# Kernel optimization log

Measured on AMD Instinct MI355X. Metric: run time of the kernel, lower is better.

Reference implementation:

```python
import jax, jax.numpy as jnp
import numpy as np

# KernelConv config (pinned by hard-coded views in the source)
KS = [1, 3, 5, 7]          # sorted kernel sizes
KTOT = sum(KS)             # 16
KMAX = KS[-1]              # 7
COLOR = 4                  # packed Bayer channels
RGB = 3
H = W = 48                 # hard-coded in source view


def setup_inputs() -> dict:
    key = jax.random.key(0)
    k1, k2, k3 = jax.random.split(key, 3)
    B, N = 4, 8
    frames = jax.random.normal(k1, (B, N, COLOR, H, W), dtype=jnp.float32)
    # core channels = N * 2*KTOT * COLOR * RGB = 8 * 32 * 12 = 3072
    core = jax.random.normal(k2, (B, N * 2 * KTOT * COLOR * RGB, H, W), dtype=jnp.float32)
    kernel_weight = jax.random.uniform(k3, (B, N, len(KS), RGB, H, W), dtype=jnp.float32)
    return {"frames": frames, "core": core, "kernel_weight": kernel_weight}


def _kernel_conv(frames, core, kernel_weight):
    B, N, color, h, w = frames.shape
    # --- _sep_conv_core: separable 1D cores -> 2D per-pixel cores (outer product) ---
    c = core.reshape(B, N, 2 * KTOT, color, RGB, h, w)
    c1, c2 = c[:, :, :KTOT], c[:, :, KTOT:]
    cores = {}
    cur = 0
    for K in KS:
        t1 = c1[:, :, cur:cur + K]          # [B,N,K,color,3,h,w]
        t2 = c2[:, :, cur:cur + K]
        # outer product over the two kernel axes (torch einsum ijklcnop,ijlmcnop->ijkmcnop)
        cores[K] = jnp.einsum('bnkcthw,bnlcthw->bnklcthw', t1, t2)  # [B,N,K,K,color,3,h,w]
        cur += K
    # --- pad all kernels to KMAX and stack (reversed kernel order, as in source) ---
    padded = []
    for K in KS[::-1]:
        p = (KMAX - K) // 2
        padded.append(jnp.pad(cores[K], ((0, 0), (0, 0), (p, p), (p, p), (0, 0), (0, 0), (0, 0), (0, 0))))
    pk = jnp.stack(padded, axis=2)                              # [B,N,S,KMAX,KMAX,color,3,h,w]
    pk = pk.reshape(B, N, len(KS), KMAX * KMAX * color, RGB, h, w)
    # weighted fusion across kernel scales
    wk = jnp.mean(pk * kernel_weight[:, :, :, None], axis=2)    # [B,N,KMAX^2*color,3,h,w]
    # --- img_stack: KMAX^2 shifted views of the padded frames ---
    r = KMAX // 2
    fpad = jnp.pad(frames, ((0, 0), (0, 0), (0, 0), (r, r), (r, r)))
    shifts = [fpad[..., i:i + h, j:j + w] for i in range(KMAX) for j in range(KMAX)]
    img_stack = jnp.stack(shifts, axis=2)                       # [B,N,KMAX^2,color,h,w]
    # --- per-pixel conv: sum over kernel taps and color for each RGB output ---
    wk_r = wk.reshape(B, N, KMAX * KMAX, color, RGB, h, w)
    pred_img_i = jnp.einsum('bnkcthw,bnkchw->bnthw', wk_r, img_stack)  # [B,N,3,h,w]
    pred_img = jnp.mean(pred_img_i, axis=1)                            # [B,3,h,w]
    return pred_img_i, pred_img


def reference(frames, core, kernel_weight):
    return _kernel_conv(frames, core, kernel_weight)
```

## Files before the change

kernel.cpp:

```cpp
#include <hip/hip_runtime.h>

#define HH 48
#define WW 48
#define HW 2304
#define NB 8
#define CB 4
#define TB 3

__global__ __launch_bounds__(256) void kconv_fused(
    const float* __restrict__ frames,
    const float* __restrict__ core,
    const float* __restrict__ kw,
    float* __restrict__ out)
{
    const int blk = blockIdx.x;
    const int pc  = blk % (HW / 64);
    int rem = blk / (HW / 64);
    const int t = rem % TB; rem /= TB;
    const int n = rem % NB;
    const int b = rem / NB;
    const int tix = threadIdx.x;
    const int c   = tix >> 6;
    const int p64 = tix & 63;
    const int pix = pc * 64 + p64;
    const int x = pix % WW;
    const int y = pix / WW;

    const float* cp = core + ((size_t)b * 3072 + (size_t)((n * 32) * CB + c) * 3 + t) * HW + pix;

    float bv[16];
    #pragma unroll
    for (int q = 0; q < 16; ++q)
        bv[q] = cp[(size_t)((q + 16) * 12) * HW];

    int   xoff[7];
    float xmsk[7];
    #pragma unroll
    for (int j = 0; j < 7; ++j) {
        const int xx = x + j - 3;
        xoff[j] = min(max(xx, 0), WW - 1);
        xmsk[j] = ((xx >= 0) & (xx < WW)) ? 1.f : 0.f;
    }

    const float* fb = frames + ((size_t)(b * NB + n) * CB + c) * HW;

    float in7[7], in5[5], in3[3], f1 = 0.f;
    #pragma unroll
    for (int i = 0; i < 7; ++i) {
        const int yy = y + i - 3;
        const float ymsk = ((yy >= 0) & (yy < HH)) ? 1.f : 0.f;
        const float* frow = fb + min(max(yy, 0), HH - 1) * WW;
        float fp[7];
        #pragma unroll
        for (int j = 0; j < 7; ++j)
            fp[j] = frow[xoff[j]] * (ymsk * xmsk[j]);
        float s7 = 0.f;
        #pragma unroll
        for (int j = 0; j < 7; ++j) s7 = fmaf(bv[9 + j], fp[j], s7);
        in7[i] = s7;
        if (i >= 1 && i <= 5) {
            float s5 = 0.f;
            #pragma unroll
            for (int j = 0; j < 5; ++j) s5 = fmaf(bv[4 + j], fp[1 + j], s5);
            in5[i - 1] = s5;
        }
        if (i >= 2 && i <= 4) {
            float s3 = 0.f;
            #pragma unroll
            for (int j = 0; j < 3; ++j) s3 = fmaf(bv[1 + j], fp[2 + j], s3);
            in3[i - 2] = s3;
        }
        if (i == 3) f1 = bv[0] * fp[3];
    }

    __builtin_amdgcn_sched_barrier(0);

    float a[16];
    #pragma unroll
    for (int q = 0; q < 16; ++q)
        a[q] = cp[(size_t)(q * 12) * HW];

    const float* kwp = kw + ((size_t)(b * NB + n) * 12 + t) * HW + pix;
    const float kw0 = kwp[0];
    const float kw1 = kwp[(size_t)3 * HW];
    const float kw2 = kwp[(size_t)6 * HW];
    const float kw3 = kwp[(size_t)9 * HW];

    float r7 = 0.f, r5 = 0.f, r3 = 0.f;
    #pragma unroll
    for (int i = 0; i < 7; ++i) r7 = fmaf(a[9 + i], in7[i], r7);
    #pragma unroll
    for (int i = 0; i < 5; ++i) r5 = fmaf(a[4 + i], in5[i], r5);
    #pragma unroll
    for (int i = 0; i < 3; ++i) r3 = fmaf(a[1 + i], in3[i], r3);
    const float r1 = a[0] * f1;

    const float val = fmaf(kw0, r7, fmaf(kw1, r5, fmaf(kw2, r3, kw3 * r1)));

    __shared__ float lds[CB][64];
    lds[c][p64] = val;
    __syncthreads();
    if (tix < 64) {
        const float s = lds[0][tix] + lds[1][tix] + lds[2][tix] + lds[3][tix];
        out[((size_t)(b * NB + n) * TB + t) * HW + pc * 64 + tix] = 0.25f * s;
    }
}

__global__ __launch_bounds__(256) void mean_fb(
    const float* __restrict__ pii, float* __restrict__ pm)
{
    const int tid = blockIdx.x * blockDim.x + threadIdx.x;
    if (tid >= 4 * TB * HW) return;
    const int pix3 = tid % (TB * HW);
    const int b = tid / (TB * HW);
    float s = 0.f;
    #pragma unroll
    for (int n = 0; n < NB; ++n)
        s += pii[(size_t)((b * NB + n) * TB) * HW + pix3];
    pm[tid] = s * 0.125f;
}

extern "C" void kernel_launch(void* const* d_in, const int* in_sizes, int n_in,
                              void* d_out, int out_size, void* d_ws, size_t ws_size,
                              hipStream_t stream) {
    const float* frames = (const float*)d_in[0];
    const float* core   = (const float*)d_in[1];
    const float* kw     = (const float*)d_in[2];
    float* out = (float*)d_out;
    float* pm  = out + 4 * NB * TB * HW;

    kconv_fused<<<4 * NB * TB * (HW / 64), 256, 0, stream>>>(frames, core, kw, out);
    mean_fb<<<(4 * TB * HW + 255) / 256, 256, 0, stream>>>(out, pm);
}
```

Before: 27.28 us.

## Fuse conv and frame-mean into one cooperative kernel with grid sync

```diff
diff --git a/kernel.cpp b/kernel.cpp
--- a/kernel.cpp
+++ b/kernel.cpp
@@ -1,4 +1,7 @@
 #include <hip/hip_runtime.h>
+#include <hip/hip_cooperative_groups.h>
+
+namespace cg = cooperative_groups;
 
 #define HH 48
 #define WW 48
@@ -6,22 +9,19 @@
 #define NB 8
 #define CB 4
 #define TB 3
+#define NCHUNK (4 * NB * TB * (HW / 64))
 
-__global__ __launch_bounds__(256) void kconv_fused(
-    const float* __restrict__ frames,
-    const float* __restrict__ core,
-    const float* __restrict__ kw,
-    float* __restrict__ out)
+
+__device__ __forceinline__ void do_chunk(
+    const float* __restrict__ frames, const float* __restrict__ core,
+    const float* __restrict__ kw, float* __restrict__ out,
+    int blk, int tix, int c, int p64, float lds[CB][64])
 {
-    const int blk = blockIdx.x;
-    const int pc  = blk % (HW / 64);
+    const int pc = blk % (HW / 64);
     int rem = blk / (HW / 64);
     const int t = rem % TB; rem /= TB;
     const int n = rem % NB;
     const int b = rem / NB;
-    const int tix = threadIdx.x;
-    const int c   = tix >> 6;
-    const int p64 = tix & 63;
     const int pix = pc * 64 + p64;
     const int x = pix % WW;
     const int y = pix / WW;
@@ -97,13 +97,48 @@
 
     const float val = fmaf(kw0, r7, fmaf(kw1, r5, fmaf(kw2, r3, kw3 * r1)));
 
-    __shared__ float lds[CB][64];
     lds[c][p64] = val;
     __syncthreads();
     if (tix < 64) {
-        const float s = lds[0][tix] + lds[1][tix] + lds[2][tix] + lds[3][tix];
-        out[((size_t)(b * NB + n) * TB + t) * HW + pc * 64 + tix] = 0.25f * s;
+        const float s4 = 0.25f * (lds[0][tix] + lds[1][tix] + lds[2][tix] + lds[3][tix]);
+        out[((size_t)(b * NB + n) * TB + t) * HW + pc * 64 + tix] = s4;
     }
+    __syncthreads();
+}
+
+__global__ __launch_bounds__(256) void kconv_coop(
+    const float* __restrict__ frames, const float* __restrict__ core,
+    const float* __restrict__ kw, float* __restrict__ out, float* __restrict__ pm)
+{
+    const int tix = threadIdx.x;
+    const int c   = tix >> 6;
+    const int p64 = tix & 63;
+    __shared__ float lds[CB][64];
+
+    for (int blk = blockIdx.x; blk < NCHUNK; blk += gridDim.x)
+        do_chunk(frames, core, kw, out, blk, tix, c, p64, lds);
+
+    cg::this_grid().sync();
+
+    for (int tid = blockIdx.x * blockDim.x + tix; tid < 4 * TB * HW;
+         tid += gridDim.x * blockDim.x) {
+        const int pix3 = tid % (TB * HW);
+        const int b = tid / (TB * HW);
+        float s = 0.f;
+        #pragma unroll
+        for (int n = 0; n < NB; ++n)
+            s += out[(size_t)((b * NB + n) * TB) * HW + pix3];
+        pm[tid] = s * 0.125f;
+    }
+}
+
+__global__ __launch_bounds__(256) void kconv_fused(
+    const float* __restrict__ frames, const float* __restrict__ core,
+    const float* __restrict__ kw, float* __restrict__ out)
+{
+    const int tix = threadIdx.x;
+    __shared__ float lds[CB][64];
+    do_chunk(frames, core, kw, out, blockIdx.x, tix, tix >> 6, tix & 63, lds);
 }
 
 __global__ __launch_bounds__(256) void mean_fb(
@@ -127,8 +162,22 @@
     const float* core   = (const float*)d_in[1];
     const float* kw     = (const float*)d_in[2];
     float* out = (float*)d_out;
-    float* pm  = out + 4 * NB * TB * HW;
+    float* pm  = out + (size_t)4 * NB * TB * HW;
 
-    kconv_fused<<<4 * NB * TB * (HW / 64), 256, 0, stream>>>(frames, core, kw, out);
+    int perCU = 0, numCU = 0, dev = 0;
+    (void)hipGetDevice(&dev);
+    hipError_t q1 = hipOccupancyMaxActiveBlocksPerMultiprocessor(&perCU, kconv_coop, 256, 0);
+    hipError_t q2 = hipDeviceGetAttribute(&numCU, hipDeviceAttributeMultiprocessorCount, dev);
+
+    if (q1 == hipSuccess && q2 == hipSuccess && perCU > 0 && numCU > 0) {
+        int grid = perCU * numCU;
+        if (grid > NCHUNK) grid = NCHUNK;
+        void* args[] = { (void*)&frames, (void*)&core, (void*)&kw, (void*)&out, (void*)&pm };
+        hipError_t le = hipLaunchCooperativeKernel((const void*)kconv_coop,
+                                                   dim3(grid), dim3(256), args, 0, stream);
+        if (le == hipSuccess) return;
+    }
+
+    kconv_fused<<<NCHUNK, 256, 0, stream>>>(frames, core, kw, out);
     mean_fb<<<(4 * TB * HW + 255) / 256, 256, 0, stream>>>(out, pm);
 }
```

Measured after the change: 97.76 us. 3.58x slower.
